# Performance work log

Measured on AMD Instinct MI355X. Metric: run time of the kernel, lower is better.

Reference implementation:

```python
import jax, jax.numpy as jnp
import numpy as np

NEG_SLOPE = 0.2  # DGL LeakyReLU default


def typed_linear(x, W, etype):
    # x: [N, in], W: [T, in, out], etype: [N] in [0, T)
    # Loop over the small fixed set of edge types (MoE-style grouped GEMM);
    # avoids gathering a [N, in, out] weight tensor.
    out = jnp.zeros((x.shape[0], W.shape[-1]), dtype=x.dtype)
    for t in range(W.shape[0]):
        out = out + jnp.where((etype == t)[:, None], x @ W[t], 0.0)
    return out


def setup_inputs() -> dict:
    key = jax.random.key(0)
    ks = jax.random.split(key, 7)
    N, IN, T, H, D = 100000, 256, 8, 16, 16
    E = 3200000
    x = jax.random.normal(ks[0], (N, IN), dtype=jnp.float32)
    W = jax.random.normal(ks[1], (T, IN, H * D), dtype=jnp.float32) * 0.05
    attn_l = jax.random.normal(ks[2], (T, H, D), dtype=jnp.float32) * 0.1
    attn_r = jax.random.normal(ks[3], (T, H, D), dtype=jnp.float32) * 0.1
    etype = jnp.sort(jax.random.randint(ks[4], (N,), 0, T, dtype=jnp.int64))
    src = jax.random.randint(ks[5], (E,), 0, N, dtype=jnp.int64)
    dst = jax.random.randint(ks[6], (E,), 0, N, dtype=jnp.int64)
    return {"x": x, "W": W, "attn_l": attn_l, "attn_r": attn_r,
            "etype": etype, "src": src, "dst": dst}


def reference(x, W, attn_l, attn_r, etype, src, dst):
    N = x.shape[0]
    T, H, D = attn_l.shape  # note H == D required by the original torch.bmm
    # TypedLinear applied once (feat_src == feat_dst in the original)
    feat = typed_linear(x, W, etype).reshape(N, H, D)
    al = attn_l[etype]  # [N, H, D]
    ar = attn_r[etype]
    # torch.bmm(feat, attn).sum(-1) == einsum('nhj,njk->nh...') summed over k
    # == feat @ attn.sum(-1)  (valid since head_size == num_heads)
    el = jnp.einsum('nhj,nj->nh', feat, al.sum(-1))  # [N, H]
    er = jnp.einsum('nhj,nj->nh', feat, ar.sum(-1))  # [N, H]
    # u_add_v over edges, then leaky relu
    e = jax.nn.leaky_relu(el[src] + er[dst], NEG_SLOPE)  # [E, H]
    # edge_softmax: softmax over incoming edges of each dst node
    m = jax.ops.segment_max(e, dst, num_segments=N)  # [N, H]
    ex = jnp.exp(e - m[dst])
    s = jax.ops.segment_sum(ex, dst, num_segments=N)  # [N, H]
    a = ex / s[dst]
    return a[..., None]  # [E, H, 1], matches el/er trailing unsqueeze
```

## Files before the change

kernel.cpp:

```cpp
#include <hip/hip_runtime.h>
#include <hip/hip_fp16.h>

#define NEG_SLOPE 0.2f

constexpr int IN_F = 256;
constexpr int NT   = 8;
constexpr int NH   = 16;
constexpr int ND   = 16;
constexpr int TM   = 32;

constexpr int NPB_SHIFT = 7;
constexpr int NPB    = 128;
constexpr int MAX_NB = 1024;
constexpr int CAP    = 4736;
constexpr int CAPB   = 6144;
constexpr int NBLK_S = 512;
constexpr int SCH    = 6272;

__global__ void precompute_w_kernel(const float* __restrict__ W,
                                    const float* __restrict__ attn_l,
                                    const float* __restrict__ attn_r,
                                    float4* __restrict__ Wc) {
    int t = blockIdx.x;
    __shared__ float alsum[NH];
    __shared__ float arsum[NH];
    int tid = threadIdx.x;
    if (tid < NH) {
        float a = 0.f, b = 0.f;
        for (int k = 0; k < ND; ++k) {
            a += attn_l[(t * NH + tid) * ND + k];
            b += attn_r[(t * NH + tid) * ND + k];
        }
        alsum[tid] = a;
        arsum[tid] = b;
    }
    __syncthreads();
    int i = tid;
    const float* wrow = W + ((size_t)t * IN_F + i) * (NH * ND);
    float sl[NH], sr[NH];
    for (int h = 0; h < NH; ++h) {
        float a = 0.f, b = 0.f;
        for (int j = 0; j < ND; ++j) {
            float w = wrow[h * ND + j];
            a += w * alsum[j];
            b += w * arsum[j];
        }
        sl[h] = a;
        sr[h] = b;
    }
    float4* dst = Wc + ((size_t)t * IN_F + i) * 8;
    for (int q = 0; q < 8; ++q) {
        float4 v;
        v.x = sl[q]; v.y = sl[q + 8]; v.z = sr[q]; v.w = sr[q + 8];
        dst[q] = v;
    }
}

__global__ __launch_bounds__(256) void node_proj_kernel(
        const float* __restrict__ x,
        const int* __restrict__ etype,
        const float4* __restrict__ Wc,
        __half* __restrict__ elh,
        float* __restrict__ er,
        int N) {
    __shared__ float4 wt[IN_F * 8];
    __shared__ int s_uni;
    __shared__ int s_t0;
    int tid = threadIdx.x;
    int n0 = blockIdx.x * TM;
    if (tid == 0) { s_t0 = etype[n0]; s_uni = 1; }
    __syncthreads();
    if (tid < TM) {
        int nn = n0 + tid;
        if (nn < N && etype[nn] != s_t0) s_uni = 0;
    }
    __syncthreads();

    int nl = tid >> 3, q = tid & 7;
    int n = n0 + nl;
    float al0 = 0.f, al1 = 0.f, ar0 = 0.f, ar1 = 0.f;

    if (s_uni) {
        const float4* wsrc = Wc + (size_t)s_t0 * IN_F * 8;
        #pragma unroll
        for (int j = 0; j < 8; ++j) wt[j * 256 + tid] = wsrc[j * 256 + tid];
        __syncthreads();
        if (n >= N) return;
        const float4* xp4 = (const float4*)(x + (size_t)n * IN_F);
        #pragma unroll 2
        for (int i4 = 0; i4 < IN_F / 4; ++i4) {
            float4 xv = xp4[i4];
            float4 w0 = wt[(i4 * 4 + 0) * 8 + q];
            float4 w1 = wt[(i4 * 4 + 1) * 8 + q];
            float4 w2 = wt[(i4 * 4 + 2) * 8 + q];
            float4 w3 = wt[(i4 * 4 + 3) * 8 + q];
            al0 += xv.x * w0.x; al1 += xv.x * w0.y; ar0 += xv.x * w0.z; ar1 += xv.x * w0.w;
            al0 += xv.y * w1.x; al1 += xv.y * w1.y; ar0 += xv.y * w1.z; ar1 += xv.y * w1.w;
            al0 += xv.z * w2.x; al1 += xv.z * w2.y; ar0 += xv.z * w2.z; ar1 += xv.z * w2.w;
            al0 += xv.w * w3.x; al1 += xv.w * w3.y; ar0 += xv.w * w3.z; ar1 += xv.w * w3.w;
        }
    } else {
        if (n >= N) return;
        int t = etype[n];
        const float4* wc = Wc + (size_t)t * IN_F * 8 + q;
        const float4* xp4 = (const float4*)(x + (size_t)n * IN_F);
        #pragma unroll 2
        for (int i4 = 0; i4 < IN_F / 4; ++i4) {
            float4 xv = xp4[i4];
            float4 w0 = wc[(size_t)(i4 * 4 + 0) * 8];
            float4 w1 = wc[(size_t)(i4 * 4 + 1) * 8];
            float4 w2 = wc[(size_t)(i4 * 4 + 2) * 8];
            float4 w3 = wc[(size_t)(i4 * 4 + 3) * 8];
            al0 += xv.x * w0.x; al1 += xv.x * w0.y; ar0 += xv.x * w0.z; ar1 += xv.x * w0.w;
            al0 += xv.y * w1.x; al1 += xv.y * w1.y; ar0 += xv.y * w1.z; ar1 += xv.y * w1.w;
            al0 += xv.z * w2.x; al1 += xv.z * w2.y; ar0 += xv.z * w2.z; ar1 += xv.z * w2.w;
            al0 += xv.w * w3.x; al1 += xv.w * w3.y; ar0 += xv.w * w3.z; ar1 += xv.w * w3.w;
        }
    }
    elh[(size_t)n * NH + q]     = __float2half(al0);
    elh[(size_t)n * NH + q + 8] = __float2half(al1);
    er[(size_t)n * NH + q]      = ar0;
    er[(size_t)n * NH + q + 8]  = ar1;
}

__global__ __launch_bounds__(512) void scatter_reserve_kernel(
        const int* __restrict__ dst,
        const int* __restrict__ src,
        int* __restrict__ cursor,
        uint2* __restrict__ packed,
        int E, int NB) {
    __shared__ unsigned short sidx[SCH];
    __shared__ int hist[MAX_NB];
    __shared__ int start_[MAX_NB];
    __shared__ int base_[MAX_NB];
    __shared__ int wsc[8];
    int tid = threadIdx.x;
    int chunk = (E + gridDim.x - 1) / gridDim.x;
    int e0 = blockIdx.x * chunk;
    int e1 = min(E, e0 + chunk);
    int cc = e1 - e0;

    for (int i = tid; i < MAX_NB; i += 512) hist[i] = 0;
    __syncthreads();
    for (int i = tid; i < cc; i += 512)
        atomicAdd(&hist[dst[e0 + i] >> NPB_SHIFT], 1);
    __syncthreads();
    for (int b = tid; b < NB; b += 512) {
        int c = hist[b];
        base_[b] = (c > 0) ? atomicAdd(&cursor[b], c) : 0;
    }
    int i0 = tid * 2;
    int c0 = hist[i0], c1 = hist[i0 + 1];
    int s2 = c0 + c1;
    int lane = tid & 63, wv = tid >> 6;
    int v = s2;
    #pragma unroll
    for (int off = 1; off < 64; off <<= 1) {
        int u = __shfl_up(v, (unsigned)off);
        v += (lane >= off) ? u : 0;
    }
    if (lane == 63) wsc[wv] = v;
    __syncthreads();
    int woff = 0;
    #pragma unroll
    for (int q = 0; q < 8; ++q) woff += (q < wv) ? wsc[q] : 0;
    int excl = woff + v - s2;
    start_[i0]     = excl;
    start_[i0 + 1] = excl + c0;
    for (int i = tid; i < MAX_NB; i += 512) hist[i] = 0;
    __syncthreads();
    for (int i = tid; i < cc; i += 512) {
        int b = dst[e0 + i] >> NPB_SHIFT;
        int lp = atomicAdd(&hist[b], 1);
        sidx[start_[b] + lp] = (unsigned short)i;
    }
    __syncthreads();
    for (int i = tid; i < cc; i += 512) {
        int le = sidx[i];
        int e = e0 + le;
        int d = dst[e];
        int b = d >> NPB_SHIFT;
        int dp = base_[b] + (i - start_[b]);
        if (dp < CAPB) {
            unsigned lo = ((unsigned)src[e] << NPB_SHIFT) | (unsigned)(d & (NPB - 1));
            unsigned long long v64 = ((unsigned long long)(unsigned)e << 32) |
                                     (unsigned long long)lo;
            __builtin_nontemporal_store(
                v64, (unsigned long long*)&packed[(size_t)b * CAPB + dp]);
        }
    }
}

__global__ __launch_bounds__(512) void bucket_sum_kernel(
        const uint2* __restrict__ packed,
        const int* __restrict__ cursor,
        const __half* __restrict__ elh,
        const float* __restrict__ er,
        float* __restrict__ out,
        int N) {
    __shared__ unsigned srt[CAP];
    __shared__ int cnt0[NPB];
    __shared__ int csum[NPB];
    __shared__ int cur[NPB];
    __shared__ float erbuf[NPB * 17];
    __shared__ float invbuf[NPB * 17];
    int b = blockIdx.x;
    int base = b << NPB_SHIFT;
    size_t off = (size_t)b * CAPB;
    int tid = threadIdx.x;
    int lane = tid & 63;
    int w = tid >> 6;
    int h = lane & 15;
    int k = lane >> 4;
    int cntb = min(cursor[b], CAPB);
    int nvalid = min(NPB, N - base);

    for (int s = tid; s < nvalid * NH; s += 512) {
        int dl = s >> 4, hh = s & 15;
        erbuf[dl * 17 + hh] = er[(size_t)(base + dl) * NH + hh];
    }

    float sacc[16];
    #pragma unroll
    for (int nn = 0; nn < 16; ++nn) sacc[nn] = 0.f;

    int nchunks = (cntb + CAP - 1) / CAP;

    for (int c = 0; c < nchunks; ++c) {
        int cbase = c * CAP;
        int cc = min(CAP, cntb - cbase);
        for (int i = tid; i < NPB; i += 512) { cnt0[i] = 0; cur[i] = 0; }
        __syncthreads();
        for (int i = tid; i < cc; i += 512)
            atomicAdd(&cnt0[packed[off + cbase + i].x & (NPB - 1)], 1);
        __syncthreads();
        if (w == 0) {
            int a  = cnt0[lane];
            int bb = cnt0[64 + lane];
            int va = a, vb = bb;
            #pragma unroll
            for (int offs = 1; offs < 64; offs <<= 1) {
                int ua = __shfl_up(va, (unsigned)offs);
                int ub = __shfl_up(vb, (unsigned)offs);
                va += (lane >= offs) ? ua : 0;
                vb += (lane >= offs) ? ub : 0;
            }
            int totA = __shfl(va, 63);
            csum[lane]      = va;
            csum[64 + lane] = vb + totA;
        }
        __syncthreads();
        for (int i = tid; i < cc; i += 512) {
            unsigned px = packed[off + cbase + i].x;
            int dl = (int)(px & (NPB - 1));
            int lp = atomicAdd(&cur[dl], 1);
            srt[csum[dl] - cnt0[dl] + lp] = px;
        }
        __syncthreads();
        #pragma unroll
        for (int nn = 0; nn < 16; ++nn) {
            int dl = w * 16 + nn;
            int m = cnt0[dl];
            if (m == 0) continue;
            int offL = csum[dl] - m;
            float erh = erbuf[dl * 17 + h];
            float s0 = 0.f, s1 = 0.f;
            int j = k;
            for (; j + 4 < m; j += 8) {
                unsigned p0 = srt[offL + j];
                unsigned p1 = srt[offL + j + 4];
                float v0 = __half2float(elh[(size_t)(p0 >> NPB_SHIFT) * NH + h]) + erh;
                float v1 = __half2float(elh[(size_t)(p1 >> NPB_SHIFT) * NH + h]) + erh;
                v0 = v0 > 0.f ? v0 : NEG_SLOPE * v0;
                v1 = v1 > 0.f ? v1 : NEG_SLOPE * v1;
                s0 += __expf(v0);
                s1 += __expf(v1);
            }
            if (j < m) {
                unsigned p0 = srt[offL + j];
                float v0 = __half2float(elh[(size_t)(p0 >> NPB_SHIFT) * NH + h]) + erh;
                v0 = v0 > 0.f ? v0 : NEG_SLOPE * v0;
                s0 += __expf(v0);
            }
            sacc[nn] += s0 + s1;
        }
        if (c + 1 < nchunks) __syncthreads();
    }

    #pragma unroll
    for (int nn = 0; nn < 16; ++nn) {
        int dl = w * 16 + nn;
        float s = sacc[nn];
        s += __shfl_xor(s, 16);
        s += __shfl_xor(s, 32);
        if (k == 0) invbuf[dl * 17 + h] = 1.0f / s;
    }
    __syncthreads();

    int i = (tid >> 4);
    for (; i + 32 < cntb; i += 64) {
        uint2 p0 = packed[off + i];
        uint2 p1 = packed[off + i + 32];
        int dl0 = (int)(p0.x & (NPB - 1)), dl1 = (int)(p1.x & (NPB - 1));
        int sid0 = (int)(p0.x >> NPB_SHIFT), sid1 = (int)(p1.x >> NPB_SHIFT);
        float v0 = __half2float(elh[(size_t)sid0 * NH + h]) + erbuf[dl0 * 17 + h];
        float v1 = __half2float(elh[(size_t)sid1 * NH + h]) + erbuf[dl1 * 17 + h];
        v0 = v0 > 0.f ? v0 : NEG_SLOPE * v0;
        v1 = v1 > 0.f ? v1 : NEG_SLOPE * v1;
        float r0 = __expf(v0) * invbuf[dl0 * 17 + h];
        float r1 = __expf(v1) * invbuf[dl1 * 17 + h];
        __builtin_nontemporal_store(r0, &out[(size_t)p0.y * NH + h]);
        __builtin_nontemporal_store(r1, &out[(size_t)p1.y * NH + h]);
    }
    if (i < cntb) {
        uint2 p0 = packed[off + i];
        int dl0 = (int)(p0.x & (NPB - 1));
        int sid0 = (int)(p0.x >> NPB_SHIFT);
        float v0 = __half2float(elh[(size_t)sid0 * NH + h]) + erbuf[dl0 * 17 + h];
        v0 = v0 > 0.f ? v0 : NEG_SLOPE * v0;
        float r0 = __expf(v0) * invbuf[dl0 * 17 + h];
        __builtin_nontemporal_store(r0, &out[(size_t)p0.y * NH + h]);
    }
}

extern "C" void kernel_launch(void* const* d_in, const int* in_sizes, int n_in,
                              void* d_out, int out_size, void* d_ws, size_t ws_size,
                              hipStream_t stream) {
    const float* x      = (const float*)d_in[0];
    const float* W      = (const float*)d_in[1];
    const float* attn_l = (const float*)d_in[2];
    const float* attn_r = (const float*)d_in[3];
    const int*   etype  = (const int*)d_in[4];
    const int*   src    = (const int*)d_in[5];
    const int*   dst    = (const int*)d_in[6];

    int N = in_sizes[4];
    int E = in_sizes[5];
    int NB = (N + NPB - 1) >> NPB_SHIFT;

    float* out = (float*)d_out;

    char* ws = (char*)d_ws;
    float4* Wc     = (float4*)ws;
    __half* elh    = (__half*)(Wc + (size_t)NT * IN_F * 8);
    float*  er     = (float*)(elh + (size_t)N * NH);
    int*    cursor = (int*)(er + (size_t)N * NH);
    uint2*  packed = (uint2*)(cursor + MAX_NB);

    hipMemsetAsync(cursor, 0, (size_t)NB * sizeof(int), stream);

    precompute_w_kernel<<<NT, 256, 0, stream>>>(W, attn_l, attn_r, Wc);

    int nb_proj = (N + TM - 1) / TM;
    node_proj_kernel<<<nb_proj, 256, 0, stream>>>(x, etype, Wc, elh, er, N);

    scatter_reserve_kernel<<<NBLK_S, 512, 0, stream>>>(dst, src, cursor, packed, E, NB);

    bucket_sum_kernel<<<NB, 512, 0, stream>>>(packed, cursor, elh, er, out, N);
}
```

Measured before the change: 217.7 us.

## Vectorize bucket softmax to head pairs and size scatter grid from edge count

Result: slower. 297.8 us (+36.8%).

```diff
diff --git a/kernel.cpp b/kernel.cpp
--- a/kernel.cpp
+++ b/kernel.cpp
@@ -14,8 +14,7 @@
 constexpr int MAX_NB = 1024;
 constexpr int CAP    = 4736;
 constexpr int CAPB   = 6144;
-constexpr int NBLK_S = 512;
-constexpr int SCH    = 6272;
+constexpr int SCH    = 3200;
 
 __global__ void precompute_w_kernel(const float* __restrict__ W,
                                     const float* __restrict__ attn_l,
@@ -139,6 +138,7 @@
     int e0 = blockIdx.x * chunk;
     int e1 = min(E, e0 + chunk);
     int cc = e1 - e0;
+    if (cc <= 0) return;
 
     for (int i = tid; i < MAX_NB; i += 512) hist[i] = 0;
     __syncthreads();
@@ -202,27 +202,27 @@
     __shared__ int cnt0[NPB];
     __shared__ int csum[NPB];
     __shared__ int cur[NPB];
-    __shared__ float erbuf[NPB * 17];
-    __shared__ float invbuf[NPB * 17];
+    __shared__ float2 erbuf2[NPB * 9];
+    __shared__ float2 invbuf2[NPB * 9];
     int b = blockIdx.x;
     int base = b << NPB_SHIFT;
     size_t off = (size_t)b * CAPB;
     int tid = threadIdx.x;
     int lane = tid & 63;
     int w = tid >> 6;
-    int h = lane & 15;
-    int k = lane >> 4;
+    int hp = lane & 7;
+    int k = lane >> 3;
     int cntb = min(cursor[b], CAPB);
     int nvalid = min(NPB, N - base);
 
-    for (int s = tid; s < nvalid * NH; s += 512) {
-        int dl = s >> 4, hh = s & 15;
-        erbuf[dl * 17 + hh] = er[(size_t)(base + dl) * NH + hh];
-    }
-
-    float sacc[16];
+    for (int s = tid; s < nvalid * 8; s += 512) {
+        int dl = s >> 3, hh = s & 7;
+        erbuf2[dl * 9 + hh] = *(const float2*)&er[(size_t)(base + dl) * NH + 2 * hh];
+    }
+
+    float2 sacc[16];
     #pragma unroll
-    for (int nn = 0; nn < 16; ++nn) sacc[nn] = 0.f;
+    for (int nn = 0; nn < 16; ++nn) { sacc[nn].x = 0.f; sacc[nn].y = 0.f; }
 
     int nchunks = (cntb + CAP - 1) / CAP;
 
@@ -263,26 +263,36 @@
             int m = cnt0[dl];
             if (m == 0) continue;
             int offL = csum[dl] - m;
-            float erh = erbuf[dl * 17 + h];
-            float s0 = 0.f, s1 = 0.f;
+            float2 er2 = erbuf2[dl * 9 + hp];
+            float s0x = 0.f, s0y = 0.f, s1x = 0.f, s1y = 0.f;
             int j = k;
-            for (; j + 4 < m; j += 8) {
+            for (; j + 8 < m; j += 16) {
                 unsigned p0 = srt[offL + j];
-                unsigned p1 = srt[offL + j + 4];
-                float v0 = __half2float(elh[(size_t)(p0 >> NPB_SHIFT) * NH + h]) + erh;
-                float v1 = __half2float(elh[(size_t)(p1 >> NPB_SHIFT) * NH + h]) + erh;
-                v0 = v0 > 0.f ? v0 : NEG_SLOPE * v0;
-                v1 = v1 > 0.f ? v1 : NEG_SLOPE * v1;
-                s0 += __expf(v0);
-                s1 += __expf(v1);
+                unsigned p1 = srt[offL + j + 8];
+                float2 f0 = __half22float2(
+                    *(const __half2*)&elh[(size_t)(p0 >> NPB_SHIFT) * NH + 2 * hp]);
+                float2 f1 = __half22float2(
+                    *(const __half2*)&elh[(size_t)(p1 >> NPB_SHIFT) * NH + 2 * hp]);
+                float v0x = f0.x + er2.x, v0y = f0.y + er2.y;
+                float v1x = f1.x + er2.x, v1y = f1.y + er2.y;
+                v0x = v0x > 0.f ? v0x : NEG_SLOPE * v0x;
+                v0y = v0y > 0.f ? v0y : NEG_SLOPE * v0y;
+                v1x = v1x > 0.f ? v1x : NEG_SLOPE * v1x;
+                v1y = v1y > 0.f ? v1y : NEG_SLOPE * v1y;
+                s0x += __expf(v0x); s0y += __expf(v0y);
+                s1x += __expf(v1x); s1y += __expf(v1y);
             }
             if (j < m) {
                 unsigned p0 = srt[offL + j];
-                float v0 = __half2float(elh[(size_t)(p0 >> NPB_SHIFT) * NH + h]) + erh;
-                v0 = v0 > 0.f ? v0 : NEG_SLOPE * v0;
-                s0 += __expf(v0);
+                float2 f0 = __half22float2(
+                    *(const __half2*)&elh[(size_t)(p0 >> NPB_SHIFT) * NH + 2 * hp]);
+                float v0x = f0.x + er2.x, v0y = f0.y + er2.y;
+                v0x = v0x > 0.f ? v0x : NEG_SLOPE * v0x;
+                v0y = v0y > 0.f ? v0y : NEG_SLOPE * v0y;
+                s0x += __expf(v0x); s0y += __expf(v0y);
             }
-            sacc[nn] += s0 + s1;
+            sacc[nn].x += s0x + s1x;
+            sacc[nn].y += s0y + s1y;
         }
         if (c + 1 < nchunks) __syncthreads();
     }
@@ -290,36 +300,56 @@
     #pragma unroll
     for (int nn = 0; nn < 16; ++nn) {
         int dl = w * 16 + nn;
-        float s = sacc[nn];
-        s += __shfl_xor(s, 16);
-        s += __shfl_xor(s, 32);
-        if (k == 0) invbuf[dl * 17 + h] = 1.0f / s;
-    }
-    __syncthreads();
-
-    int i = (tid >> 4);
-    for (; i + 32 < cntb; i += 64) {
+        float sx = sacc[nn].x, sy = sacc[nn].y;
+        sx += __shfl_xor(sx, 8);  sy += __shfl_xor(sy, 8);
+        sx += __shfl_xor(sx, 16); sy += __shfl_xor(sy, 16);
+        sx += __shfl_xor(sx, 32); sy += __shfl_xor(sy, 32);
+        if (k == 0) {
+            float2 iv; iv.x = 1.0f / sx; iv.y = 1.0f / sy;
+            invbuf2[dl * 9 + hp] = iv;
+        }
+    }
+    __syncthreads();
+
+    int i = (tid >> 3);
+    for (; i + 64 < cntb; i += 128) {
         uint2 p0 = packed[off + i];
-        uint2 p1 = packed[off + i + 32];
+        uint2 p1 = packed[off + i + 64];
         int dl0 = (int)(p0.x & (NPB - 1)), dl1 = (int)(p1.x & (NPB - 1));
-        int sid0 = (int)(p0.x >> NPB_SHIFT), sid1 = (int)(p1.x >> NPB_SHIFT);
-        float v0 = __half2float(elh[(size_t)sid0 * NH + h]) + erbuf[dl0 * 17 + h];
-        float v1 = __half2float(elh[(size_t)sid1 * NH + h]) + erbuf[dl1 * 17 + h];
-        v0 = v0 > 0.f ? v0 : NEG_SLOPE * v0;
-        v1 = v1 > 0.f ? v1 : NEG_SLOPE * v1;
-        float r0 = __expf(v0) * invbuf[dl0 * 17 + h];
-        float r1 = __expf(v1) * invbuf[dl1 * 17 + h];
-        __builtin_nontemporal_store(r0, &out[(size_t)p0.y * NH + h]);
-        __builtin_nontemporal_store(r1, &out[(size_t)p1.y * NH + h]);
+        float2 f0 = __half22float2(
+            *(const __half2*)&elh[(size_t)(p0.x >> NPB_SHIFT) * NH + 2 * hp]);
+        float2 f1 = __half22float2(
+            *(const __half2*)&elh[(size_t)(p1.x >> NPB_SHIFT) * NH + 2 * hp]);
+        float2 e0 = erbuf2[dl0 * 9 + hp], e1 = erbuf2[dl1 * 9 + hp];
+        float2 i0 = invbuf2[dl0 * 9 + hp], i1 = invbuf2[dl1 * 9 + hp];
+        float v0x = f0.x + e0.x, v0y = f0.y + e0.y;
+        float v1x = f1.x + e1.x, v1y = f1.y + e1.y;
+        v0x = v0x > 0.f ? v0x : NEG_SLOPE * v0x;
+        v0y = v0y > 0.f ? v0y : NEG_SLOPE * v0y;
+        v1x = v1x > 0.f ? v1x : NEG_SLOPE * v1x;
+        v1y = v1y > 0.f ? v1y : NEG_SLOPE * v1y;
+        union { float f[2]; unsigned long long u; } pk0, pk1;
+        pk0.f[0] = __expf(v0x) * i0.x; pk0.f[1] = __expf(v0y) * i0.y;
+        pk1.f[0] = __expf(v1x) * i1.x; pk1.f[1] = __expf(v1y) * i1.y;
+        __builtin_nontemporal_store(
+            pk0.u, (unsigned long long*)&out[(size_t)p0.y * NH + 2 * hp]);
+        __builtin_nontemporal_store(
+            pk1.u, (unsigned long long*)&out[(size_t)p1.y * NH + 2 * hp]);
     }
     if (i < cntb) {
         uint2 p0 = packed[off + i];
         int dl0 = (int)(p0.x & (NPB - 1));
-        int sid0 = (int)(p0.x >> NPB_SHIFT);
-        float v0 = __half2float(elh[(size_t)sid0 * NH + h]) + erbuf[dl0 * 17 + h];
-        v0 = v0 > 0.f ? v0 : NEG_SLOPE * v0;
-        float r0 = __expf(v0) * invbuf[dl0 * 17 + h];
-        __builtin_nontemporal_store(r0, &out[(size_t)p0.y * NH + h]);
+        float2 f0 = __half22float2(
+            *(const __half2*)&elh[(size_t)(p0.x >> NPB_SHIFT) * NH + 2 * hp]);
+        float2 e0 = erbuf2[dl0 * 9 + hp];
+        float2 i0 = invbuf2[dl0 * 9 + hp];
+        float v0x = f0.x + e0.x, v0y = f0.y + e0.y;
+        v0x = v0x > 0.f ? v0x : NEG_SLOPE * v0x;
+        v0y = v0y > 0.f ? v0y : NEG_SLOPE * v0y;
+        union { float f[2]; unsigned long long u; } pk0;
+        pk0.f[0] = __expf(v0x) * i0.x; pk0.f[1] = __expf(v0y) * i0.y;
+        __builtin_nontemporal_store(
+            pk0.u, (unsigned long long*)&out[(size_t)p0.y * NH + 2 * hp]);
     }
 }
 
@@ -354,7 +384,8 @@
     int nb_proj = (N + TM - 1) / TM;
     node_proj_kernel<<<nb_proj, 256, 0, stream>>>(x, etype, Wc, elh, er, N);
 
-    scatter_reserve_kernel<<<NBLK_S, 512, 0, stream>>>(dst, src, cursor, packed, E, NB);
+    int nblk_s = (E + SCH - 1) / SCH;
+    scatter_reserve_kernel<<<nblk_s, 512, 0, stream>>>(dst, src, cursor, packed, E, NB);
 
     bucket_sum_kernel<<<NB, 512, 0, stream>>>(packed, cursor, elh, er, out, N);
 }
```
